# Kernel tuning notes

Hardware: AMD Instinct MI355X
Metric: run time of the kernel (lower is better)

Reference implementation:

```python
import jax, jax.numpy as jnp
import numpy as np

B, S, D, V, L = 8, 8192, 768, 64, 26  # batch, seq, hidden, symbol vocab, labels


def setup_inputs() -> dict:
    key = jax.random.key(0)
    k1, k2, k3 = jax.random.split(key, 3)
    hidden_states = jax.random.normal(k1, (B, S, D), dtype=jnp.float32)
    input_ids = jax.random.randint(k2, (B, S), 0, V, dtype=jnp.int32)
    W = jax.random.normal(k3, (L, D), dtype=jnp.float32) * 0.02
    b = jnp.zeros((L,), dtype=jnp.float32)
    return {"hidden_states": hidden_states, "W": W, "b": b, "input_ids": input_ids}


def reference(hidden_states, W, b, input_ids):
    # Per-batch, per-symbol mean pooling of hidden states, then linear classify.
    # Dense/padded equivalent of the torch per-symbol boolean-mask loop:
    # row (batch_b, symbol_v) = classifier(mean of hidden_states[b] where input_ids[b]==v),
    # masked to 0 for symbol 0 and for symbols absent in the sequence.
    Bv, Sv, Dv = hidden_states.shape
    seg = (input_ids + jnp.arange(Bv, dtype=input_ids.dtype)[:, None] * V).reshape(-1)
    flat_h = hidden_states.reshape(-1, Dv)
    sums = jax.ops.segment_sum(flat_h, seg, num_segments=Bv * V)            # [B*V, D]
    counts = jax.ops.segment_sum(
        jnp.ones((Bv * Sv,), dtype=hidden_states.dtype), seg, num_segments=Bv * V
    )                                                                        # [B*V]
    means = sums / jnp.maximum(counts, 1.0)[:, None]
    logits = means @ W.T + b                                                 # [B*V, L]
    present = (counts > 0) & ((jnp.arange(Bv * V) % V) > 0)                  # exclude symbol 0
    logits = jnp.where(present[:, None], logits, 0.0)
    return logits.reshape(Bv, V, -1)
```

## Files before the change

### kernel.cpp

```cpp
#include <hip/hip_runtime.h>

#define B_ 8
#define S_ 8192
#define D_ 768
#define V_ 64
#define L_ 26

typedef __attribute__((ext_vector_type(8))) short short8;
typedef __attribute__((ext_vector_type(4))) float floatx4;

#define TOKS 512
#define SLICES (S_ / TOKS)
#define NSL  48
#define KSTEPS (TOKS / 32)

__device__ __forceinline__ void load_kstep(
    const float* __restrict__ hrow, const int* __restrict__ idrow,
    int kk, int quad, int nl, float (&f)[3][8], int4& i0, int4& i1)
{
    const int kb = kk * 32 + quad * 8;
    const int4* ip = (const int4*)(idrow + kb);
    i0 = ip[0]; i1 = ip[1];
    #pragma unroll
    for (int nt = 0; nt < 3; ++nt) {
        const float* bp = hrow + (size_t)kb * D_ + nt * 16 + nl;
        #pragma unroll
        for (int j = 0; j < 8; ++j) f[nt][j] = bp[(size_t)j * D_];
    }
}

__device__ __forceinline__ void compute_kstep(
    const float (&f)[3][8], int4 i0, int4 i1, int nl, floatx4 (&acc)[4][3])
{
    const int idv[8] = {i0.x, i0.y, i0.z, i0.w, i1.x, i1.y, i1.z, i1.w};

    short8 afrag[4];
    #pragma unroll
    for (int j = 0; j < 8; ++j) {
        const int id  = idv[j];
        const short e = ((id & 15) == nl) ? (short)0x3F80 : (short)0;
        const int hi4 = id >> 4;
        #pragma unroll
        for (int mt = 0; mt < 4; ++mt)
            afrag[mt][j] = (hi4 == mt) ? e : (short)0;
    }

    #pragma unroll
    for (int nt = 0; nt < 3; ++nt) {
        short8 bhi, blo;
        #pragma unroll
        for (int j = 0; j < 8; ++j) {
            const unsigned u = __builtin_bit_cast(unsigned, f[nt][j]);
            bhi[j] = (short)(u >> 16);
            const float hif = __builtin_bit_cast(float, u & 0xFFFF0000u);
            const float lof = f[nt][j] - hif;
            blo[j] = (short)(__builtin_bit_cast(unsigned, lof) >> 16);
        }
        #pragma unroll
        for (int mt = 0; mt < 4; ++mt) {
            acc[mt][nt] = __builtin_amdgcn_mfma_f32_16x16x32_bf16(
                afrag[mt], bhi, acc[mt][nt], 0, 0, 0);
            acc[mt][nt] = __builtin_amdgcn_mfma_f32_16x16x32_bf16(
                afrag[mt], blo, acc[mt][nt], 0, 0, 0);
        }
    }
}

__global__ __launch_bounds__(256, 2) void pool_mfma_kernel(
    const float* __restrict__ h, const int* __restrict__ ids,
    float* __restrict__ part, unsigned int* __restrict__ cntpart)
{
    __shared__ unsigned int cnt[V_];

    const int tid  = threadIdx.x;
    const int lane = tid & 63;
    const int wave = tid >> 6;
    const int nl   = lane & 15;
    const int quad = lane >> 4;

    const int b     = blockIdx.z;
    const int slice = blockIdx.x;
    const int k0    = slice * TOKS;
    const int n0    = blockIdx.y * (4 * NSL) + wave * NSL;

    const int*   idrow = ids + b * S_ + k0;
    const float* hrow  = h + ((size_t)b * S_ + k0) * D_ + n0;

    if (blockIdx.y == 0) {
        if (tid < V_) cnt[tid] = 0u;
        __syncthreads();
        if (tid < TOKS / 4) {
            const int4 q = ((const int4*)idrow)[tid];
            atomicAdd(&cnt[q.x], 1u); atomicAdd(&cnt[q.y], 1u);
            atomicAdd(&cnt[q.z], 1u); atomicAdd(&cnt[q.w], 1u);
        }
        __syncthreads();
        if (tid < V_) cntpart[(slice * B_ + b) * V_ + tid] = cnt[tid];
    }

    floatx4 acc[4][3];
    #pragma unroll
    for (int mt = 0; mt < 4; ++mt)
        #pragma unroll
        for (int nt = 0; nt < 3; ++nt) acc[mt][nt] = (floatx4)0.f;

    float fA[3][8], fB[3][8];
    int4 iA0, iA1, iB0, iB1;
    load_kstep(hrow, idrow, 0, quad, nl, fA, iA0, iA1);
    #pragma unroll
    for (int ks = 0; ks < KSTEPS; ks += 2) {
        load_kstep(hrow, idrow, ks + 1, quad, nl, fB, iB0, iB1);
        compute_kstep(fA, iA0, iA1, nl, acc);
        if (ks + 2 < KSTEPS)
            load_kstep(hrow, idrow, ks + 2, quad, nl, fA, iA0, iA1);
        compute_kstep(fB, iB0, iB1, nl, acc);
    }

    float* pbase = part + ((size_t)(slice * B_ + b) * V_) * D_;
    #pragma unroll
    for (int mt = 0; mt < 4; ++mt)
        #pragma unroll
        for (int nt = 0; nt < 3; ++nt)
            #pragma unroll
            for (int r = 0; r < 4; ++r) {
                const int v = mt * 16 + quad * 4 + r;
                const int d = n0 + nt * 16 + nl;
                pbase[(size_t)v * D_ + d] = acc[mt][nt][r];
            }
}

__global__ __launch_bounds__(256) void reduce_finalize_kernel(
    const float* __restrict__ part, const unsigned int* __restrict__ cntpart,
    const float* __restrict__ Wm, const float* __restrict__ bias,
    float* __restrict__ out)
{
    __shared__ float mean[D_];
    __shared__ unsigned int scnt;

    const int tid = threadIdx.x;
    const int bv  = blockIdx.x;
    const int b   = bv >> 6;
    const int v   = bv & (V_ - 1);

    if (tid == 0) scnt = 0u;
    __syncthreads();
    if (tid < SLICES)
        atomicAdd(&scnt, cntpart[(tid * B_ + b) * V_ + v]);

    floatx4 s4 = (floatx4)0.f;
    if (tid < D_ / 4) {
        #pragma unroll
        for (int sl = 0; sl < SLICES; ++sl) {
            const floatx4 p4 = *(const floatx4*)
                &part[((size_t)(sl * B_ + b) * V_ + v) * D_ + 4 * tid];
            s4 += p4;
        }
    }
    __syncthreads();
    const unsigned int c = scnt;
    const float inv = 1.f / (float)(c > 1u ? c : 1u);
    if (tid < D_ / 4) {
        #pragma unroll
        for (int x = 0; x < 4; ++x) mean[4 * tid + x] = s4[x] * inv;
    }
    __syncthreads();

    const bool present = (c > 0u) && (v > 0);
    const int lane = tid & 63;
    const int wave = tid >> 6;
    for (int l = wave; l < L_; l += 4) {
        const float* wrow = Wm + l * D_;
        float p = 0.f;
        #pragma unroll
        for (int j = 0; j < 12; ++j) {
            const int d = lane + 64 * j;
            p += mean[d] * wrow[d];
        }
        #pragma unroll
        for (int off = 32; off > 0; off >>= 1) p += __shfl_down(p, off);
        if (lane == 0) out[bv * L_ + l] = present ? (p + bias[l]) : 0.f;
    }
}

extern "C" void kernel_launch(void* const* d_in, const int* in_sizes, int n_in,
                              void* d_out, int out_size, void* d_ws, size_t ws_size,
                              hipStream_t stream) {
    const float* h    = (const float*)d_in[0];
    const float* Wm   = (const float*)d_in[1];
    const float* bias = (const float*)d_in[2];
    const int*   ids  = (const int*)d_in[3];
    float* out = (float*)d_out;

    float* part = (float*)d_ws;
    unsigned int* cntpart =
        (unsigned int*)(part + (size_t)SLICES * B_ * V_ * D_);

    dim3 grid1(SLICES, D_ / (4 * NSL), B_);
    pool_mfma_kernel<<<grid1, 256, 0, stream>>>(h, ids, part, cntpart);

    reduce_finalize_kernel<<<B_ * V_, 256, 0, stream>>>(
        part, cntpart, Wm, bias, out);
}
```

Baseline: 296.5 us.

## Stage hidden-state tiles through LDS with async global_load_lds double buffering

```diff
diff --git a/kernel.cpp b/kernel.cpp
--- a/kernel.cpp
+++ b/kernel.cpp
@@ -12,22 +12,10 @@
 #define TOKS 512
 #define SLICES (S_ / TOKS)
 #define NSL  48
+#define BLKN (4 * NSL)
 #define KSTEPS (TOKS / 32)
-
-__device__ __forceinline__ void load_kstep(
-    const float* __restrict__ hrow, const int* __restrict__ idrow,
-    int kk, int quad, int nl, float (&f)[3][8], int4& i0, int4& i1)
-{
-    const int kb = kk * 32 + quad * 8;
-    const int4* ip = (const int4*)(idrow + kb);
-    i0 = ip[0]; i1 = ip[1];
-    #pragma unroll
-    for (int nt = 0; nt < 3; ++nt) {
-        const float* bp = hrow + (size_t)kb * D_ + nt * 16 + nl;
-        #pragma unroll
-        for (int j = 0; j < 8; ++j) f[nt][j] = bp[(size_t)j * D_];
-    }
-}
+#define TILE_FLOATS (32 * BLKN)
+#define CH_PER_THREAD 6
 
 __device__ __forceinline__ void compute_kstep(
     const float (&f)[3][8], int4 i0, int4 i1, int nl, floatx4 (&acc)[4][3])
@@ -70,6 +58,8 @@
     const float* __restrict__ h, const int* __restrict__ ids,
     float* __restrict__ part, unsigned int* __restrict__ cntpart)
 {
+    __shared__ __align__(16) float tile[2][TILE_FLOATS];
+    __shared__ __align__(16) int ids_lds[TOKS];
     __shared__ unsigned int cnt[V_];
 
     const int tid  = threadIdx.x;
@@ -81,39 +71,79 @@
     const int b     = blockIdx.z;
     const int slice = blockIdx.x;
     const int k0    = slice * TOKS;
-    const int n0    = blockIdx.y * (4 * NSL) + wave * NSL;
-
-    const int*   idrow = ids + b * S_ + k0;
-    const float* hrow  = h + ((size_t)b * S_ + k0) * D_ + n0;
+    const int n0    = blockIdx.y * BLKN + wave * NSL;
+
+    const int*  idrow = ids + b * S_ + k0;
+    const char* hblk  = (const char*)
+        (h + ((size_t)b * S_ + k0) * D_ + blockIdx.y * BLKN);
+
+    int goff[CH_PER_THREAD];
+    #pragma unroll
+    for (int t = 0; t < CH_PER_THREAD; ++t) {
+        const int C   = (t * 4 + wave) * 64 + lane;
+        const int row = C / 48;
+        const int c16 = C % 48;
+        goff[t] = row * (D_ * 4) + c16 * 16;
+    }
+
+    if (wave == 0) {
+        #pragma unroll
+        for (int i = 0; i < 2; ++i)
+            __builtin_amdgcn_global_load_lds(
+                (const unsigned int*)(idrow + i * 256 + lane * 4),
+                (unsigned int*)&ids_lds[i * 256], 16, 0, 0);
+    }
+    #pragma unroll
+    for (int t = 0; t < CH_PER_THREAD; ++t)
+        __builtin_amdgcn_global_load_lds(
+            (const unsigned int*)(hblk + goff[t]),
+            (unsigned int*)&tile[0][(t * 4 + wave) * 256], 16, 0, 0);
+
+    __syncthreads();
+
+    floatx4 acc[4][3];
+    #pragma unroll
+    for (int mt = 0; mt < 4; ++mt)
+        #pragma unroll
+        for (int nt = 0; nt < 3; ++nt) acc[mt][nt] = (floatx4)0.f;
+
+    #pragma unroll 2
+    for (int ks = 0; ks < KSTEPS; ++ks) {
+        if (ks + 1 < KSTEPS) {
+            const char* gs = hblk + (ks + 1) * (32 * D_ * 4);
+            #pragma unroll
+            for (int t = 0; t < CH_PER_THREAD; ++t)
+                __builtin_amdgcn_global_load_lds(
+                    (const unsigned int*)(gs + goff[t]),
+                    (unsigned int*)&tile[(ks + 1) & 1][(t * 4 + wave) * 256],
+                    16, 0, 0);
+        }
+
+        const float* tb = &tile[ks & 1][0];
+        const int kb = ks * 32 + quad * 8;
+        const int4 i0 = *(const int4*)&ids_lds[kb];
+        const int4 i1 = *(const int4*)&ids_lds[kb + 4];
+        float f[3][8];
+        #pragma unroll
+        for (int nt = 0; nt < 3; ++nt)
+            #pragma unroll
+            for (int j = 0; j < 8; ++j)
+                f[nt][j] = tb[(quad * 8 + j) * BLKN + wave * NSL + nt * 16 + nl];
+        compute_kstep(f, i0, i1, nl, acc);
+
+        __syncthreads();
+    }
 
     if (blockIdx.y == 0) {
         if (tid < V_) cnt[tid] = 0u;
         __syncthreads();
         if (tid < TOKS / 4) {
-            const int4 q = ((const int4*)idrow)[tid];
+            const int4 q = *(const int4*)&ids_lds[tid * 4];
             atomicAdd(&cnt[q.x], 1u); atomicAdd(&cnt[q.y], 1u);
             atomicAdd(&cnt[q.z], 1u); atomicAdd(&cnt[q.w], 1u);
         }
         __syncthreads();
         if (tid < V_) cntpart[(slice * B_ + b) * V_ + tid] = cnt[tid];
-    }
-
-    floatx4 acc[4][3];
-    #pragma unroll
-    for (int mt = 0; mt < 4; ++mt)
-        #pragma unroll
-        for (int nt = 0; nt < 3; ++nt) acc[mt][nt] = (floatx4)0.f;
-
-    float fA[3][8], fB[3][8];
-    int4 iA0, iA1, iB0, iB1;
-    load_kstep(hrow, idrow, 0, quad, nl, fA, iA0, iA1);
-    #pragma unroll
-    for (int ks = 0; ks < KSTEPS; ks += 2) {
-        load_kstep(hrow, idrow, ks + 1, quad, nl, fB, iB0, iB1);
-        compute_kstep(fA, iA0, iA1, nl, acc);
-        if (ks + 2 < KSTEPS)
-            load_kstep(hrow, idrow, ks + 2, quad, nl, fA, iA0, iA1);
-        compute_kstep(fB, iB0, iB1, nl, acc);
     }
 
     float* pbase = part + ((size_t)(slice * B_ + b) * V_) * D_;
@@ -195,7 +225,7 @@
     unsigned int* cntpart =
         (unsigned int*)(part + (size_t)SLICES * B_ * V_ * D_);
 
-    dim3 grid1(SLICES, D_ / (4 * NSL), B_);
+    dim3 grid1(SLICES, D_ / BLKN, B_);
     pool_mfma_kernel<<<grid1, 256, 0, stream>>>(h, ids, part, cntpart);
 
     reduce_finalize_kernel<<<B_ * V_, 256, 0, stream>>>(
```

Measured after the change: 289.5 us (median of 2 runs). 2.4% less time.
